# Performance work log

Hardware: AMD Instinct MI355X
Metric: run time of the kernel (lower is better)

Reference implementation:

```python
import jax, jax.numpy as jnp
import numpy as np

B, I, H, O = 4096, 1024, 2048, 512  # batch, input_size, experts_out(hidden), experts_hidden(output)
E_SPEC, E_SH = 4, 4


def _experts(x, W1, b1, W2, b2):
    # x:[B,I], W1:[E,I,H], b1:[E,H], W2:[E,H,O], b2:[E,O] -> [E,B,O]
    # Expert: fc2(dropout(relu(fc1(x)))); dropout is identity in eval mode.
    h = jax.nn.relu(jnp.einsum('bi,eih->ebh', x, W1) + b1[:, None, :])
    return jnp.einsum('ebh,eho->ebo', h, W2) + b2[:, None, :]


def setup_inputs() -> dict:
    key = jax.random.key(0)
    ks = jax.random.split(key, 32)
    s = 0.02
    d = {}
    d['x_shared'] = jax.random.normal(ks[0], (B, I), jnp.float32)
    d['x_task1'] = jax.random.normal(ks[1], (B, I), jnp.float32)
    d['x_task2'] = jax.random.normal(ks[2], (B, I), jnp.float32)
    # expert params for shared / task1 / task2 groups
    for n, (grp, kbase) in enumerate([('sh', 3), ('t1', 8), ('t2', 13)]):
        E = E_SH if grp == 'sh' else E_SPEC
        d[f'w1_{grp}'] = jax.random.normal(ks[kbase], (E, I, H), jnp.float32) * s
        d[f'b1_{grp}'] = jnp.zeros((E, H), jnp.float32)
        d[f'w2_{grp}'] = jax.random.normal(ks[kbase + 1], (E, H, O), jnp.float32) * s
        d[f'b2_{grp}'] = jnp.zeros((E, O), jnp.float32)
    # gate params
    d['wg_sh'] = jax.random.normal(ks[20], (I, 2 * E_SPEC + E_SH), jnp.float32) * s
    d['bg_sh'] = jnp.zeros((2 * E_SPEC + E_SH,), jnp.float32)
    d['wg_t1'] = jax.random.normal(ks[21], (I, E_SPEC + E_SH), jnp.float32) * s
    d['bg_t1'] = jnp.zeros((E_SPEC + E_SH,), jnp.float32)
    d['wg_t2'] = jax.random.normal(ks[22], (I, E_SPEC + E_SH), jnp.float32) * s
    d['bg_t2'] = jnp.zeros((E_SPEC + E_SH,), jnp.float32)
    return d


def reference(x_shared, x_task1, x_task2,
              w1_sh, b1_sh, w2_sh, b2_sh,
              w1_t1, b1_t1, w2_t1, b2_t1,
              w1_t2, b1_t2, w2_t2, b2_t2,
              wg_sh, bg_sh, wg_t1, bg_t1, wg_t2, bg_t2):
    sh_o = _experts(x_shared, w1_sh, b1_sh, w2_sh, b2_sh)  # [Esh,B,O]
    t1_o = _experts(x_task1, w1_t1, b1_t1, w2_t1, b2_t1)   # [Esp,B,O]
    t2_o = _experts(x_task2, w1_t2, b1_t2, w2_t2, b2_t2)   # [Esp,B,O]

    g1 = jax.nn.softmax(x_task1 @ wg_t1 + bg_t1, axis=1)    # [B,Esp+Esh]
    g2 = jax.nn.softmax(x_task2 @ wg_t2 + bg_t2, axis=1)
    gs = jax.nn.softmax(x_shared @ wg_sh + bg_sh, axis=1)   # [B,2Esp+Esh]

    out1 = jnp.einsum('ebc,be->bc', jnp.concatenate([t1_o, sh_o], 0), g1)
    out2 = jnp.einsum('ebc,be->bc', jnp.concatenate([t2_o, sh_o], 0), g2)
    out_sh = jnp.einsum('ebc,be->bc', jnp.concatenate([t1_o, t2_o, sh_o], 0), gs)
    # if_last=False -> return [shared, task1, task2]
    return (out_sh, out1, out2)
```

## Files before the change

kernel.cpp:

```cpp
#include <hip/hip_runtime.h>

#define B_DIM 4096
#define I_DIM 1024
#define H_DIM 2048
#define O_DIM 512

typedef unsigned short ushort_t;
typedef unsigned long long ull_t;
typedef __attribute__((ext_vector_type(4))) float f32x4;
typedef __attribute__((ext_vector_type(8))) short bf16x8;
typedef __attribute__((ext_vector_type(8))) unsigned short u16x8;
typedef __attribute__((ext_vector_type(4))) unsigned short u16x4;

__device__ __forceinline__ unsigned short f2bf(float f) {
  union { float f; unsigned int u; } v; v.f = f;
  unsigned int u = v.u;
  u += 0x7fffu + ((u >> 16) & 1u);
  return (unsigned short)(u >> 16);
}
__device__ __forceinline__ float bf2f(unsigned short h) {
  union { unsigned int u; float f; } v; v.u = ((unsigned int)h) << 16;
  return v.f;
}

__device__ __forceinline__ void gld16(const void* g, void* l) {
  __builtin_amdgcn_global_load_lds(
      (const __attribute__((address_space(1))) unsigned int*)((ull_t)g),
      (__attribute__((address_space(3))) unsigned int*)((unsigned int)(ull_t)l),
      16, 0, 0);
}

__device__ __forceinline__ int swz_off(int row, int col) {
  int off = ((((row >> 4) << 1) + (col >> 5)) << 10) + ((row & 15) << 6) + ((col & 31) << 1);
  off ^= ((row >> 3) & 1) << 5;
  return off;
}

template <bool RELU>
__device__ __forceinline__ void gemm_core_256(
    const ushort_t* __restrict__ A,
    const ushort_t* __restrict__ Bt,
    const float*    __restrict__ bias,
    ushort_t*       __restrict__ C,
    int N, int K, int bm0, int bn0)
{
  __shared__ __align__(16) ushort_t sh[2][2][16384];

  const int tid  = threadIdx.x;
  const int lane = tid & 63;
  const int wave = tid >> 6;
  const int wm = wave >> 2, wn = wave & 3;
  const int r16 = lane & 15, kq = lane >> 4;

  int   loff[4];
  ull_t goffA[4], goffB[4];
#pragma unroll
  for (int r = 0; r < 4; ++r) {
    const int L = (r * 512 + tid) * 16;
    const int P = L ^ (((L >> 9) & 1) << 5);
    const int s = P >> 10;
    const int row = ((s >> 1) << 4) | ((P >> 6) & 15);
    const int col = ((s & 1) << 5) | (((P >> 4) & 3) << 3);
    loff[r]  = L;
    goffA[r] = (ull_t)(bm0 + row) * K + col;
    goffB[r] = (ull_t)(bn0 + row) * K + col;
  }
  const int NT = K >> 6;

  int offA[8][2], offB[4][2];
#pragma unroll
  for (int m = 0; m < 8; ++m)
#pragma unroll
    for (int ks = 0; ks < 2; ++ks)
      offA[m][ks] = swz_off(wm * 128 + m * 16 + r16, ks * 32 + kq * 8);
#pragma unroll
  for (int n = 0; n < 4; ++n)
#pragma unroll
    for (int ks = 0; ks < 2; ++ks)
      offB[n][ks] = swz_off(wn * 64 + n * 16 + r16, ks * 32 + kq * 8);

  f32x4 acc[8][4] = {};

  auto stage = [&](int b, int kt) {
    const int k0 = kt << 6;
    char* baseA = (char*)&sh[b][0][0];
    char* baseB = (char*)&sh[b][1][0];
#pragma unroll
    for (int r = 0; r < 4; ++r) gld16(A + goffA[r] + k0, baseA + loff[r]);
#pragma unroll
    for (int r = 0; r < 4; ++r) gld16(Bt + goffB[r] + k0, baseB + loff[r]);
  };

  stage(0, 0);
  stage(1, 1);

  for (int kt = 0; kt < NT; ++kt) {
    const int b = kt & 1;
    if (kt == NT - 1) asm volatile("s_waitcnt vmcnt(0)" ::: "memory");
    else              asm volatile("s_waitcnt vmcnt(8)" ::: "memory");
    __builtin_amdgcn_s_barrier();
    asm volatile("" ::: "memory");

    const char* tA = (const char*)&sh[b][0][0];
    const char* tB = (const char*)&sh[b][1][0];

    bf16x8 a0[4][2], a1[4][2], bf0[2][2], bf1[2][2];
#pragma unroll
    for (int m = 0; m < 4; ++m) {
      a0[m][0] = *(const bf16x8*)(tA + offA[m][0]);
      a0[m][1] = *(const bf16x8*)(tA + offA[m][1]);
    }
#pragma unroll
    for (int n = 0; n < 2; ++n) {
      bf0[n][0] = *(const bf16x8*)(tB + offB[n][0]);
      bf0[n][1] = *(const bf16x8*)(tB + offB[n][1]);
    }
    __builtin_amdgcn_s_setprio(1);
#pragma unroll
    for (int m = 0; m < 4; ++m)
#pragma unroll
      for (int n = 0; n < 2; ++n)
#pragma unroll
        for (int ks = 0; ks < 2; ++ks)
          acc[m][n] = __builtin_amdgcn_mfma_f32_16x16x32_bf16(a0[m][ks], bf0[n][ks], acc[m][n], 0, 0, 0);
    __builtin_amdgcn_s_setprio(0);
#pragma unroll
    for (int n = 0; n < 2; ++n) {
      bf1[n][0] = *(const bf16x8*)(tB + offB[n + 2][0]);
      bf1[n][1] = *(const bf16x8*)(tB + offB[n + 2][1]);
    }
    __builtin_amdgcn_s_setprio(1);
#pragma unroll
    for (int m = 0; m < 4; ++m)
#pragma unroll
      for (int n = 0; n < 2; ++n)
#pragma unroll
        for (int ks = 0; ks < 2; ++ks)
          acc[m][n + 2] = __builtin_amdgcn_mfma_f32_16x16x32_bf16(a0[m][ks], bf1[n][ks], acc[m][n + 2], 0, 0, 0);
    __builtin_amdgcn_s_setprio(0);
#pragma unroll
    for (int m = 0; m < 4; ++m) {
      a1[m][0] = *(const bf16x8*)(tA + offA[m + 4][0]);
      a1[m][1] = *(const bf16x8*)(tA + offA[m + 4][1]);
    }
    __builtin_amdgcn_s_setprio(1);
#pragma unroll
    for (int m = 0; m < 4; ++m)
#pragma unroll
      for (int n = 0; n < 2; ++n)
#pragma unroll
        for (int ks = 0; ks < 2; ++ks)
          acc[m + 4][n + 2] = __builtin_amdgcn_mfma_f32_16x16x32_bf16(a1[m][ks], bf1[n][ks], acc[m + 4][n + 2], 0, 0, 0);
    __builtin_amdgcn_s_setprio(0);
    __builtin_amdgcn_s_setprio(1);
#pragma unroll
    for (int m = 0; m < 4; ++m)
#pragma unroll
      for (int n = 0; n < 2; ++n)
#pragma unroll
        for (int ks = 0; ks < 2; ++ks)
          acc[m + 4][n] = __builtin_amdgcn_mfma_f32_16x16x32_bf16(a1[m][ks], bf0[n][ks], acc[m + 4][n], 0, 0, 0);
    __builtin_amdgcn_s_setprio(0);

    asm volatile("" ::: "memory");
    __builtin_amdgcn_s_barrier();
    if (kt + 2 < NT) stage(b, kt + 2);
  }

  float bv[4];
#pragma unroll
  for (int n = 0; n < 4; ++n) bv[n] = bias[bn0 + wn * 64 + n * 16 + r16];
#pragma unroll
  for (int m = 0; m < 8; ++m) {
    const int row = bm0 + wm * 128 + m * 16 + kq * 4;
#pragma unroll
    for (int n = 0; n < 4; ++n) {
      const int col = bn0 + wn * 64 + n * 16 + r16;
#pragma unroll
      for (int j = 0; j < 4; ++j) {
        float v = acc[m][n][j] + bv[n];
        if (RELU) v = fmaxf(v, 0.f);
        C[(ull_t)(row + j) * N + col] = f2bf(v);
      }
    }
  }
}

__device__ __forceinline__ void xcd_swz(int& bx, int& by, int& bz) {
  const int gx = gridDim.x, gy = gridDim.y;
  const int total = gx * gy * gridDim.z;
  const int flat = blockIdx.x + gx * (blockIdx.y + gy * blockIdx.z);
  const int q = total >> 3;
  const int s = (flat & 7) * q + (flat >> 3);
  bx = s % gx;
  const int rest = s / gx;
  by = rest % gy;
  bz = rest / gy;
}

__global__ __launch_bounds__(512, 2) void gemm1_256_kernel(
    const ushort_t* __restrict__ xb,
    const ushort_t* __restrict__ w1t,
    const float* __restrict__ b1_t1, const float* __restrict__ b1_t2, const float* __restrict__ b1_sh,
    ushort_t* __restrict__ hbuf,
    int ebase)
{
  int bx, by, bz; xcd_swz(bx, by, bz);
  const int eg = ebase + bz;
  const ushort_t* A  = xb + (ull_t)(eg >> 2) * B_DIM * I_DIM;
  const ushort_t* Bt = w1t + (ull_t)bz * H_DIM * I_DIM;
  const float* bias = (eg < 4 ? b1_t1 : eg < 8 ? b1_t2 : b1_sh) + (ull_t)(eg & 3) * H_DIM;
  ushort_t* C = hbuf + (ull_t)bz * B_DIM * H_DIM;
  gemm_core_256<true>(A, Bt, bias, C, H_DIM, I_DIM, by * 256, bx * 256);
}

__global__ __launch_bounds__(512, 2) void gemm2_256_kernel(
    const ushort_t* __restrict__ hbuf,
    const ushort_t* __restrict__ w2t,
    const float* __restrict__ b2_t1, const float* __restrict__ b2_t2, const float* __restrict__ b2_sh,
    ushort_t* __restrict__ eout,
    int ebase)
{
  int bx, by, bz; xcd_swz(bx, by, bz);
  const int eg = ebase + bz;
  const ushort_t* A  = hbuf + (ull_t)bz * B_DIM * H_DIM;
  const ushort_t* Bt = w2t + (ull_t)bz * O_DIM * H_DIM;
  const float* bias = (eg < 4 ? b2_t1 : eg < 8 ? b2_t2 : b2_sh) + (ull_t)(eg & 3) * O_DIM;
  ushort_t* C = eout + (ull_t)eg * B_DIM * O_DIM;
  gemm_core_256<false>(A, Bt, bias, C, O_DIM, H_DIM, by * 256, bx * 256);
}

__global__ void tcast_kernel(const float* __restrict__ s_t1, const float* __restrict__ s_t2,
                             const float* __restrict__ s_sh, ushort_t* __restrict__ dst,
                             int R, int C, int ebase)
{
  __shared__ float tile[32][33];
  const int eg = ebase + blockIdx.z;
  const float* src = (eg < 4 ? s_t1 : eg < 8 ? s_t2 : s_sh) + (ull_t)(eg & 3) * R * C;
  ushort_t* d = dst + (ull_t)blockIdx.z * R * C;
  const int tx = threadIdx.x, ty = threadIdx.y;
  const int r0 = blockIdx.y * 32, c0 = blockIdx.x * 32;
#pragma unroll
  for (int i = 0; i < 32; i += 8)
    tile[ty + i][tx] = src[(ull_t)(r0 + ty + i) * C + c0 + tx];
  __syncthreads();
#pragma unroll
  for (int i = 0; i < 32; i += 8)
    d[(ull_t)(c0 + ty + i) * R + r0 + tx] = f2bf(tile[tx][ty + i]);
}

__global__ void cast_x_kernel(const float* __restrict__ xt1, const float* __restrict__ xt2,
                              const float* __restrict__ xsh, ushort_t* __restrict__ dst)
{
  const int slot = blockIdx.y;
  const float* src = slot == 0 ? xt1 : slot == 1 ? xt2 : xsh;
  const ull_t base = ((ull_t)blockIdx.x * 256 + threadIdx.x) * 8;
  const f32x4* s4 = (const f32x4*)(src + base);
  f32x4 a = s4[0], b = s4[1];
  u16x8 r;
  r[0] = f2bf(a[0]); r[1] = f2bf(a[1]); r[2] = f2bf(a[2]); r[3] = f2bf(a[3]);
  r[4] = f2bf(b[0]); r[5] = f2bf(b[1]); r[6] = f2bf(b[2]); r[7] = f2bf(b[3]);
  *(u16x8*)(dst + (ull_t)slot * B_DIM * I_DIM + base) = r;
}

__global__ void prep_gates_w_kernel(const float* __restrict__ wg_sh, const float* __restrict__ wg_t1,
                                    const float* __restrict__ wg_t2, ushort_t* __restrict__ wgtb)
{
  const int t = blockIdx.x;
  const float* src = t == 0 ? wg_sh : t == 1 ? wg_t1 : wg_t2;
  const int n = t == 0 ? 12 : 8;
  ushort_t* dst = wgtb + (ull_t)t * 16 * I_DIM;
  for (int i = threadIdx.x; i < 16 * (I_DIM / 8); i += blockDim.x) {
    const int c = i >> 7, j0 = (i & 127) * 8;
    u16x8 r;
#pragma unroll
    for (int k = 0; k < 8; ++k)
      r[k] = (c < n) ? f2bf(src[(ull_t)(j0 + k) * n + c]) : (ushort_t)0;
    *(u16x8*)(dst + (ull_t)c * I_DIM + j0) = r;
  }
}

__global__ __launch_bounds__(256, 2) void gates_mfma_kernel(
    const ushort_t* __restrict__ xb, const ushort_t* __restrict__ wgtb,
    const float* __restrict__ bg_sh, const float* __restrict__ bg_t1, const float* __restrict__ bg_t2,
    float* __restrict__ gates)
{
  __shared__ __align__(16) ushort_t As[128 * 32];
  const int task = blockIdx.y;
  const int slot = task == 0 ? 2 : task - 1;
  const int n = task == 0 ? 12 : 8;
  const float* bg = task == 0 ? bg_sh : task == 1 ? bg_t1 : bg_t2;
  float* out = task == 0 ? gates
             : task == 1 ? gates + (ull_t)B_DIM * 12
                         : gates + (ull_t)B_DIM * 20;
  const ushort_t* A  = xb + (ull_t)slot * B_DIM * I_DIM;
  const ushort_t* Bt = wgtb + (ull_t)task * 16 * I_DIM;

  const int tid = threadIdx.x, lane = tid & 63, wave = tid >> 6;
  const int brow = blockIdx.x * 128;
  const int r16 = lane & 15, kq = lane >> 4;

  f32x4 acc[2] = {};
  const int c0 = tid, c1 = tid + 256;
  const ull_t a_off0 = (ull_t)(brow + (c0 >> 2)) * I_DIM + (c0 & 3) * 8;
  const ull_t a_off1 = (ull_t)(brow + (c1 >> 2)) * I_DIM + (c1 & 3) * 8;

  for (int k0 = 0; k0 < I_DIM; k0 += 32) {
    gld16(A + a_off0 + k0, As + c0 * 8);
    gld16(A + a_off1 + k0, As + c1 * 8);
    __syncthreads();
    const bf16x8 bfr = *(const bf16x8*)(Bt + (ull_t)r16 * I_DIM + k0 + kq * 8);
    const bf16x8 af0 = *(const bf16x8*)(As + (wave * 32 + r16) * 32 + kq * 8);
    const bf16x8 af1 = *(const bf16x8*)(As + (wave * 32 + 16 + r16) * 32 + kq * 8);
    acc[0] = __builtin_amdgcn_mfma_f32_16x16x32_bf16(af0, bfr, acc[0], 0, 0, 0);
    acc[1] = __builtin_amdgcn_mfma_f32_16x16x32_bf16(af1, bfr, acc[1], 0, 0, 0);
    __syncthreads();
  }

  const float bv = (r16 < n) ? bg[r16] : 0.f;
#pragma unroll
  for (int m = 0; m < 2; ++m) {
#pragma unroll
    for (int j = 0; j < 4; ++j) {
      float v = (r16 < n) ? (acc[m][j] + bv) : -1e30f;
      float mx = v;
#pragma unroll
      for (int d = 1; d < 16; d <<= 1) mx = fmaxf(mx, __shfl_xor(mx, d));
      const float e = __expf(v - mx);
      float s = e;
#pragma unroll
      for (int d = 1; d < 16; d <<= 1) s += __shfl_xor(s, d);
      const int row = brow + wave * 32 + m * 16 + kq * 4 + j;
      if (r16 < n) out[(ull_t)row * n + r16] = e / s;
    }
  }
}

__global__ __launch_bounds__(256) void combine_kernel(
    const ushort_t* __restrict__ eout, const float* __restrict__ gates, float* __restrict__ out)
{
  const ull_t idx4 = (ull_t)blockIdx.x * 256 + threadIdx.x;
  const int b  = (int)(idx4 >> 7);
  const int o4 = ((int)idx4 & 127) * 4;
  const float* gs = gates + (ull_t)b * 12;
  const float* g1 = gates + (ull_t)B_DIM * 12 + (ull_t)b * 8;
  const float* g2 = gates + (ull_t)B_DIM * 20 + (ull_t)b * 8;
  float osh[4] = {0, 0, 0, 0}, o1[4] = {0, 0, 0, 0}, o2[4] = {0, 0, 0, 0};
#pragma unroll
  for (int j = 0; j < 12; ++j) {
    const u16x4 ev = *(const u16x4*)(eout + ((ull_t)j * B_DIM + b) * O_DIM + o4);
    const float wsh = gs[j];
    const float w1 = (j < 4) ? g1[j] : (j >= 8 ? g1[j - 4] : 0.f);
    const float w2 = (j < 4) ? 0.f : g2[j - 4];
#pragma unroll
    for (int t = 0; t < 4; ++t) {
      const float e = bf2f(ev[t]);
      osh[t] += wsh * e; o1[t] += w1 * e; o2[t] += w2 * e;
    }
  }
  const ull_t nBO = (ull_t)B_DIM * O_DIM;
  const ull_t obase = (ull_t)b * O_DIM + o4;
  f32x4 v0 = {osh[0], osh[1], osh[2], osh[3]};
  f32x4 v1 = {o1[0], o1[1], o1[2], o1[3]};
  f32x4 v2 = {o2[0], o2[1], o2[2], o2[3]};
  *(f32x4*)(out + obase) = v0;
  *(f32x4*)(out + nBO + obase) = v1;
  *(f32x4*)(out + 2 * nBO + obase) = v2;
}

extern "C" void kernel_launch(void* const* d_in, const int* in_sizes, int n_in,
                              void* d_out, int out_size, void* d_ws, size_t ws_size,
                              hipStream_t stream)
{
  const float* x_sh  = (const float*)d_in[0];
  const float* x_t1  = (const float*)d_in[1];
  const float* x_t2  = (const float*)d_in[2];
  const float* w1_sh = (const float*)d_in[3];
  const float* b1_sh = (const float*)d_in[4];
  const float* w2_sh = (const float*)d_in[5];
  const float* b2_sh = (const float*)d_in[6];
  const float* w1_t1 = (const float*)d_in[7];
  const float* b1_t1 = (const float*)d_in[8];
  const float* w2_t1 = (const float*)d_in[9];
  const float* b2_t1 = (const float*)d_in[10];
  const float* w1_t2 = (const float*)d_in[11];
  const float* b1_t2 = (const float*)d_in[12];
  const float* w2_t2 = (const float*)d_in[13];
  const float* b2_t2 = (const float*)d_in[14];
  const float* wg_sh = (const float*)d_in[15];
  const float* bg_sh = (const float*)d_in[16];
  const float* wg_t1 = (const float*)d_in[17];
  const float* bg_t1 = (const float*)d_in[18];
  const float* wg_t2 = (const float*)d_in[19];
  const float* bg_t2 = (const float*)d_in[20];

  char* p = (char*)d_ws;
  auto alloc = [&](size_t bytes) { char* r = p; p += (bytes + 255) & ~(size_t)255; return r; };

  ushort_t* xb    = (ushort_t*)alloc(3ull * B_DIM * I_DIM * 2);
  ushort_t* eout  = (ushort_t*)alloc(12ull * B_DIM * O_DIM * 2);
  float*    gates = (float*)alloc(28ull * B_DIM * 4);
  ushort_t* wgtb  = (ushort_t*)alloc(3ull * 16 * I_DIM * 2);

  const size_t used_fixed = (size_t)(p - (char*)d_ws);
  const size_t per_e = ((size_t)H_DIM * I_DIM + (size_t)O_DIM * H_DIM + (size_t)B_DIM * H_DIM) * 2 + 3 * 256;
  int eb = 1;
  if (ws_size > used_fixed + per_e) eb = (int)((ws_size - used_fixed) / per_e);
  if (eb > 12) eb = 12;
  if (eb < 1)  eb = 1;

  ushort_t* w1t  = (ushort_t*)alloc((size_t)eb * H_DIM * I_DIM * 2);
  ushort_t* w2t  = (ushort_t*)alloc((size_t)eb * O_DIM * H_DIM * 2);
  ushort_t* hbuf = (ushort_t*)alloc((size_t)eb * B_DIM * H_DIM * 2);

  cast_x_kernel<<<dim3(2048, 3), 256, 0, stream>>>(x_t1, x_t2, x_sh, xb);
  prep_gates_w_kernel<<<3, 256, 0, stream>>>(wg_sh, wg_t1, wg_t2, wgtb);
  gates_mfma_kernel<<<dim3(B_DIM / 128, 3), 256, 0, stream>>>(xb, wgtb, bg_sh, bg_t1, bg_t2, gates);
  for (int ebase = 0; ebase < 12; ebase += eb) {
    const int cnt = (12 - ebase < eb) ? (12 - ebase) : eb;
    tcast_kernel<<<dim3(H_DIM / 32, I_DIM / 32, cnt), dim3(32, 8), 0, stream>>>(
        w1_t1, w1_t2, w1_sh, w1t, I_DIM, H_DIM, ebase);
    tcast_kernel<<<dim3(O_DIM / 32, H_DIM / 32, cnt), dim3(32, 8), 0, stream>>>(
        w2_t1, w2_t2, w2_sh, w2t, H_DIM, O_DIM, ebase);
    gemm1_256_kernel<<<dim3(H_DIM / 256, B_DIM / 256, cnt), 512, 0, stream>>>(
        xb, w1t, b1_t1, b1_t2, b1_sh, hbuf, ebase);
    gemm2_256_kernel<<<dim3(O_DIM / 256, B_DIM / 256, cnt), 512, 0, stream>>>(
        hbuf, w2t, b2_t1, b2_t2, b2_sh, eout, ebase);
  }
  combine_kernel<<<dim3((B_DIM * O_DIM / 4) / 256), 256, 0, stream>>>(eout, gates, (float*)d_out);
}
```

Measured before the change: 459.7 us.

## Interleave global prefetch with MFMA phases using ping-pong barriers in GEMM loop

Splits tile staging into separate A and B loads and issues the next-next tile's B and A prefetches mid-iteration, as soon as the corresponding LDS fragments have been read, instead of at the loop end. Adds workgroup barriers and lgkmcnt waits with sched_barriers between each LDS-read and MFMA phase to lock waves into a ping-pong schedule. The aim is to overlap global-to-LDS traffic with matrix math. The cost is many more barriers per iteration, which may stall waves.

```diff
diff --git a/kernel.cpp b/kernel.cpp
--- a/kernel.cpp
+++ b/kernel.cpp
@@ -81,30 +81,34 @@
 
   f32x4 acc[8][4] = {};
 
-  auto stage = [&](int b, int kt) {
+  auto stageA = [&](int b, int kt) {
     const int k0 = kt << 6;
     char* baseA = (char*)&sh[b][0][0];
+#pragma unroll
+    for (int r = 0; r < 4; ++r) gld16(A + goffA[r] + k0, baseA + loff[r]);
+  };
+  auto stageB = [&](int b, int kt) {
+    const int k0 = kt << 6;
     char* baseB = (char*)&sh[b][1][0];
-#pragma unroll
-    for (int r = 0; r < 4; ++r) gld16(A + goffA[r] + k0, baseA + loff[r]);
 #pragma unroll
     for (int r = 0; r < 4; ++r) gld16(Bt + goffB[r] + k0, baseB + loff[r]);
   };
 
-  stage(0, 0);
-  stage(1, 1);
+  stageA(0, 0); stageB(0, 0);
+  stageA(1, 1); stageB(1, 1);
 
   for (int kt = 0; kt < NT; ++kt) {
     const int b = kt & 1;
-    if (kt == NT - 1) asm volatile("s_waitcnt vmcnt(0)" ::: "memory");
-    else              asm volatile("s_waitcnt vmcnt(8)" ::: "memory");
-    __builtin_amdgcn_s_barrier();
-    asm volatile("" ::: "memory");
+    const bool pre = (kt + 2 < NT);
+    if (kt < NT - 1) asm volatile("s_waitcnt vmcnt(8)" ::: "memory");
+    else             asm volatile("s_waitcnt vmcnt(0)" ::: "memory");
+    __builtin_amdgcn_s_barrier();
 
     const char* tA = (const char*)&sh[b][0][0];
     const char* tB = (const char*)&sh[b][1][0];
 
     bf16x8 a0[4][2], a1[4][2], bf0[2][2], bf1[2][2];
+
 #pragma unroll
     for (int m = 0; m < 4; ++m) {
       a0[m][0] = *(const bf16x8*)(tA + offA[m][0]);
@@ -115,6 +119,10 @@
       bf0[n][0] = *(const bf16x8*)(tB + offB[n][0]);
       bf0[n][1] = *(const bf16x8*)(tB + offB[n][1]);
     }
+    asm volatile("" ::: "memory");
+    __builtin_amdgcn_s_barrier();
+    asm volatile("s_waitcnt lgkmcnt(0)" ::: "memory");
+    __builtin_amdgcn_sched_barrier(0);
     __builtin_amdgcn_s_setprio(1);
 #pragma unroll
     for (int m = 0; m < 4; ++m)
@@ -124,11 +132,18 @@
         for (int ks = 0; ks < 2; ++ks)
           acc[m][n] = __builtin_amdgcn_mfma_f32_16x16x32_bf16(a0[m][ks], bf0[n][ks], acc[m][n], 0, 0, 0);
     __builtin_amdgcn_s_setprio(0);
+    asm volatile("" ::: "memory");
+    __builtin_amdgcn_s_barrier();
+
 #pragma unroll
     for (int n = 0; n < 2; ++n) {
       bf1[n][0] = *(const bf16x8*)(tB + offB[n + 2][0]);
       bf1[n][1] = *(const bf16x8*)(tB + offB[n + 2][1]);
     }
+    asm volatile("" ::: "memory");
+    __builtin_amdgcn_s_barrier();
+    asm volatile("s_waitcnt lgkmcnt(0)" ::: "memory");
+    __builtin_amdgcn_sched_barrier(0);
     __builtin_amdgcn_s_setprio(1);
 #pragma unroll
     for (int m = 0; m < 4; ++m)
@@ -138,11 +153,19 @@
         for (int ks = 0; ks < 2; ++ks)
           acc[m][n + 2] = __builtin_amdgcn_mfma_f32_16x16x32_bf16(a0[m][ks], bf1[n][ks], acc[m][n + 2], 0, 0, 0);
     __builtin_amdgcn_s_setprio(0);
+    asm volatile("" ::: "memory");
+    __builtin_amdgcn_s_barrier();
+
 #pragma unroll
     for (int m = 0; m < 4; ++m) {
       a1[m][0] = *(const bf16x8*)(tA + offA[m + 4][0]);
       a1[m][1] = *(const bf16x8*)(tA + offA[m + 4][1]);
     }
+    if (pre) stageB(b, kt + 2);
+    asm volatile("" ::: "memory");
+    __builtin_amdgcn_s_barrier();
+    asm volatile("s_waitcnt lgkmcnt(0)" ::: "memory");
+    __builtin_amdgcn_sched_barrier(0);
     __builtin_amdgcn_s_setprio(1);
 #pragma unroll
     for (int m = 0; m < 4; ++m)
@@ -152,6 +175,13 @@
         for (int ks = 0; ks < 2; ++ks)
           acc[m + 4][n + 2] = __builtin_amdgcn_mfma_f32_16x16x32_bf16(a1[m][ks], bf1[n][ks], acc[m + 4][n + 2], 0, 0, 0);
     __builtin_amdgcn_s_setprio(0);
+    asm volatile("" ::: "memory");
+    __builtin_amdgcn_s_barrier();
+
+    if (pre) stageA(b, kt + 2);
+    asm volatile("" ::: "memory");
+    __builtin_amdgcn_s_barrier();
+    __builtin_amdgcn_sched_barrier(0);
     __builtin_amdgcn_s_setprio(1);
 #pragma unroll
     for (int m = 0; m < 4; ++m)
@@ -161,10 +191,8 @@
         for (int ks = 0; ks < 2; ++ks)
           acc[m + 4][n] = __builtin_amdgcn_mfma_f32_16x16x32_bf16(a1[m][ks], bf0[n][ks], acc[m + 4][n], 0, 0, 0);
     __builtin_amdgcn_s_setprio(0);
-
-    asm volatile("" ::: "memory");
-    __builtin_amdgcn_s_barrier();
-    if (kt + 2 < NT) stage(b, kt + 2);
+    asm volatile("" ::: "memory");
+    __builtin_amdgcn_s_barrier();
   }
 
   float bv[4];
```

Measured after the change: 443.2 us. 1.04x faster.
